# Kernel optimization log

Measured on AMD Instinct MI355X. Metric: run time of the kernel, lower is better.

The kernel has to match this reference:

```python
import jax, jax.numpy as jnp
import numpy as np

# 8 trilerp corners in (x, y, z) component order, matching the original's
# [floor/ceil] enumeration: fff, ffc, fcf, fcc, cff, cfc, ccf, ccc.
CORNERS = np.array([[0, 0, 0], [0, 0, 1], [0, 1, 0], [0, 1, 1],
                    [1, 0, 0], [1, 0, 1], [1, 1, 0], [1, 1, 1]], dtype=np.int32)

N = 32768          # number of points
NUM_KERNELS = 4    # submodels
GRID = 16          # voxel grid size
C_IN = 64          # input_channels
C_OUT = 64         # features


def setup_inputs() -> dict:
    key = jax.random.key(0)
    k1, k2, k3, k4, k5 = jax.random.split(key, 5)
    param_idxs = jax.random.randint(k1, (N, 1), 0, NUM_KERNELS, dtype=jnp.int32)
    pos = jax.random.uniform(k2, (N, 3), dtype=jnp.float32)
    xs = jax.random.normal(k3, (N, C_IN), dtype=jnp.float32)
    # he_uniform over fan_in = input_channels
    limit = np.sqrt(6.0 / C_IN).astype(np.float32)
    kernels = jax.random.uniform(
        k4, (NUM_KERNELS, GRID, GRID, GRID, C_IN, C_OUT),
        dtype=jnp.float32, minval=-limit, maxval=limit)
    biases = jnp.zeros((NUM_KERNELS, GRID, GRID, GRID, C_OUT), dtype=jnp.float32)
    return {"param_idxs": param_idxs, "pos": pos, "xs": xs,
            "kernels": kernels, "biases": biases}


def reference(param_idxs, pos, xs, kernels, biases):
    """Trilinearly-interpolated per-point dense layer.

    Equivalent to building kernel = sum_c w_c * K_c and computing x @ kernel + bias;
    by linearity we accumulate w_c * (x @ K_c + b_c) directly, avoiding the
    materialized per-point interpolated kernel.
    """
    grid = kernels.shape[1]
    pidx = param_idxs.reshape(-1)            # (N,)
    loc = pos * grid - 0.5                    # (N, 3)
    floored = jnp.floor(loc)
    ceil_w = loc - floored                    # trilerp weights toward ceil
    floor_w = 1.0 - ceil_w
    out = jnp.zeros((pos.shape[0], kernels.shape[-1]), dtype=xs.dtype)
    for corner in CORNERS:                    # fixed 8-iteration loop
        idx = jnp.clip((floored + corner).astype(jnp.int32), 0, grid - 1)  # (N,3)
        w = jnp.prod(jnp.where(corner[None, :] == 1, ceil_w, floor_w), axis=-1)  # (N,)
        # Original indexes kernels[pidx, z, y, x] with z=idx[:,2], y=idx[:,1], x=idx[:,0]
        gk = kernels[pidx, idx[:, 2], idx[:, 1], idx[:, 0]]  # (N, C_in, C_out)
        gb = biases[pidx, idx[:, 2], idx[:, 1], idx[:, 0]]   # (N, C_out)
        out = out + w[:, None] * (jnp.einsum('nc,ncf->nf', xs, gk) + gb)
    return out
```

## Files before the change

kernel.cpp:

```cpp
#include <hip/hip_runtime.h>
#include <math.h>

#define NPTS   32768
#define NK     4
#define GRID_  16
#define CIN    64
#define COUT   64
#define NCELLS (NK*GRID_*GRID_*GRID_)
#define NENT   (NPTS*8)
#define NENTP  (NENT + NCELLS*15)
#define CPB    16

typedef __attribute__((ext_vector_type(8))) short  short8;
typedef __attribute__((ext_vector_type(4))) float  f32x4;

static __device__ inline unsigned short f2bf(float f) {
    unsigned int u = __builtin_bit_cast(unsigned int, f);
    unsigned int r = u + 0x7fff + ((u >> 16) & 1);
    return (unsigned short)(r >> 16);
}

__global__ void k_hist(const int* __restrict__ pidx, const float* __restrict__ pos,
                       int* __restrict__ hist, int n) {
    int p = blockIdx.x * blockDim.x + threadIdx.x;
    if (p >= n) return;
    int pk = pidx[p];
    float lx = pos[3*p+0]*16.f - 0.5f;
    float ly = pos[3*p+1]*16.f - 0.5f;
    float lz = pos[3*p+2]*16.f - 0.5f;
    int fx = (int)floorf(lx), fy = (int)floorf(ly), fz = (int)floorf(lz);
#pragma unroll
    for (int c = 0; c < 8; ++c) {
        int c0 = c & 1, c1 = (c >> 1) & 1, c2 = (c >> 2) & 1;
        int ix = min(max(fx + c0, 0), GRID_-1);
        int iy = min(max(fy + c1, 0), GRID_-1);
        int iz = min(max(fz + c2, 0), GRID_-1);
        int cell = ((pk*GRID_ + iz)*GRID_ + iy)*GRID_ + ix;
        atomicAdd(&hist[cell], 1);
    }
}

__global__ void k_alloc(const int* __restrict__ hist, int* __restrict__ offsets,
                        int* __restrict__ cursor, int* __restrict__ gcnt) {
    int i = blockIdx.x * blockDim.x + threadIdx.x;
    int l = threadIdx.x & 63;
    int v  = hist[i];
    int vp = (v + 15) & ~15;
    int p = vp;
#pragma unroll
    for (int d = 1; d < 64; d <<= 1) {
        int t = __shfl_up(p, d);
        if (l >= d) p += t;
    }
    int total = __shfl(p, 63);
    int base = 0;
    if (l == 63) base = atomicAdd(gcnt, total);
    base = __shfl(base, 63);
    int off = base + p - vp;
    offsets[i] = off;
    cursor[i]  = off;
}

__global__ void k_scatter(const int* __restrict__ pidx, const float* __restrict__ pos,
                          int* __restrict__ cursor, int* __restrict__ epid,
                          float* __restrict__ ew, int n) {
    int p = blockIdx.x * blockDim.x + threadIdx.x;
    if (p >= n) return;
    int pk = pidx[p];
    float lx = pos[3*p+0]*16.f - 0.5f;
    float ly = pos[3*p+1]*16.f - 0.5f;
    float lz = pos[3*p+2]*16.f - 0.5f;
    float flx = floorf(lx), fly = floorf(ly), flz = floorf(lz);
    int fx = (int)flx, fy = (int)fly, fz = (int)flz;
    float tx = lx - flx, ty = ly - fly, tz = lz - flz;
    float wx[2] = {1.f - tx, tx};
    float wy[2] = {1.f - ty, ty};
    float wz[2] = {1.f - tz, tz};
#pragma unroll
    for (int c = 0; c < 8; ++c) {
        int c0 = c & 1, c1 = (c >> 1) & 1, c2 = (c >> 2) & 1;
        int ix = min(max(fx + c0, 0), GRID_-1);
        int iy = min(max(fy + c1, 0), GRID_-1);
        int iz = min(max(fz + c2, 0), GRID_-1);
        int cell = ((pk*GRID_ + iz)*GRID_ + iy)*GRID_ + ix;
        float w = wx[c0] * wy[c1] * wz[c2];
        int e = atomicAdd(&cursor[cell], 1);
        epid[e] = p;
        ew[e]   = w;
    }
}

__global__ __launch_bounds__(256)
void k_main(const float* __restrict__ xs, const float* __restrict__ kernels,
            const float* __restrict__ biases, const int* __restrict__ offsets,
            const int* __restrict__ hist, const int* __restrict__ epid,
            const float* __restrict__ ew, float* __restrict__ out) {
    __shared__ float Ks[2][CIN * COUT];
    int tid = threadIdx.x;
    int l   = tid & 63;
    int wv  = tid >> 6;
    int m16 = l & 15;
    int q   = l >> 4;
    int cell0 = blockIdx.x * CPB;
    int ncol  = wv * 16 + m16;

    {
        const float* Kg = kernels + (size_t)cell0 * (CIN * COUT);
#pragma unroll
        for (int r = 0; r < 4; ++r) {
            int off = ((r * 4 + wv) * 64 + l) * 4;
            __builtin_amdgcn_global_load_lds(
                (const __attribute__((address_space(1))) void*)(Kg + off),
                (__attribute__((address_space(3))) void*)(&Ks[0][off]), 16, 0, 0);
        }
    }

    for (int ci = 0; ci < CPB; ++ci) {
        int cur = ci & 1;
        __syncthreads();
        if (ci + 1 < CPB) {
            const float* Kg = kernels + (size_t)(cell0 + ci + 1) * (CIN * COUT);
#pragma unroll
            for (int r = 0; r < 4; ++r) {
                int off = ((r * 4 + wv) * 64 + l) * 4;
                __builtin_amdgcn_global_load_lds(
                    (const __attribute__((address_space(1))) void*)(Kg + off),
                    (__attribute__((address_space(3))) void*)(&Ks[1 - cur][off]), 16, 0, 0);
            }
        }
        int cell = cell0 + ci;
        int cnt  = hist[cell];
        if (cnt == 0) continue;
        int start = offsets[cell];

        short8 Bf0, Bf1;
#pragma unroll
        for (int j = 0; j < 8; ++j) {
            Bf0[j] = (short)f2bf(Ks[cur][(q * 8 + j) * COUT + ncol]);
            Bf1[j] = (short)f2bf(Ks[cur][(32 + q * 8 + j) * COUT + ncol]);
        }
        float bias_c = biases[(size_t)cell * COUT + ncol];

        int nb = (cnt + 15) >> 4;
        for (int b = 0; b < nb; ++b) {
            int ebase = start + (b << 4);
            int pidA = epid[ebase + m16] & (NPTS - 1);
            const float* xr = xs + (size_t)pidA * CIN + q * 8;
            float4 a0 = *(const float4*)(xr);
            float4 a1 = *(const float4*)(xr + 4);
            float4 a2 = *(const float4*)(xr + 32);
            float4 a3 = *(const float4*)(xr + 36);
            short8 af0, af1;
            af0[0]=(short)f2bf(a0.x); af0[1]=(short)f2bf(a0.y);
            af0[2]=(short)f2bf(a0.z); af0[3]=(short)f2bf(a0.w);
            af0[4]=(short)f2bf(a1.x); af0[5]=(short)f2bf(a1.y);
            af0[6]=(short)f2bf(a1.z); af0[7]=(short)f2bf(a1.w);
            af1[0]=(short)f2bf(a2.x); af1[1]=(short)f2bf(a2.y);
            af1[2]=(short)f2bf(a2.z); af1[3]=(short)f2bf(a2.w);
            af1[4]=(short)f2bf(a3.x); af1[5]=(short)f2bf(a3.y);
            af1[6]=(short)f2bf(a3.z); af1[7]=(short)f2bf(a3.w);

            f32x4 acc = {0.f, 0.f, 0.f, 0.f};
            acc = __builtin_amdgcn_mfma_f32_16x16x32_bf16(af0, Bf0, acc, 0, 0, 0);
            acc = __builtin_amdgcn_mfma_f32_16x16x32_bf16(af1, Bf1, acc, 0, 0, 0);

            int erow = ebase + (q << 2);
            int4   pe = *(const int4*)&epid[erow];
            float4 we = *(const float4*)&ew[erow];
            int rem = cnt - (b << 4) - (q << 2);
            if (rem > 0) {
                unsafeAtomicAdd(&out[(size_t)(pe.x) * COUT + ncol], we.x * (acc[0] + bias_c));
                if (rem > 1) unsafeAtomicAdd(&out[(size_t)(pe.y) * COUT + ncol], we.y * (acc[1] + bias_c));
                if (rem > 2) unsafeAtomicAdd(&out[(size_t)(pe.z) * COUT + ncol], we.z * (acc[2] + bias_c));
                if (rem > 3) unsafeAtomicAdd(&out[(size_t)(pe.w) * COUT + ncol], we.w * (acc[3] + bias_c));
            }
        }
    }
}

extern "C" void kernel_launch(void* const* d_in, const int* in_sizes, int n_in,
                              void* d_out, int out_size, void* d_ws, size_t ws_size,
                              hipStream_t stream) {
    const int*   pidx    = (const int*)  d_in[0];
    const float* pos     = (const float*)d_in[1];
    const float* xs      = (const float*)d_in[2];
    const float* kernels = (const float*)d_in[3];
    const float* biases  = (const float*)d_in[4];
    float*       out     = (float*)d_out;
    int n = in_sizes[0];

    int* ws      = (int*)d_ws;
    int* hist    = ws;
    int* gcnt    = ws + NCELLS;
    int* offsets = ws + NCELLS + 16;
    int* cursor  = offsets + NCELLS;
    int* epid    = cursor + NCELLS;
    float* ew    = (float*)(epid + NENTP);

    hipMemsetAsync(hist, 0, (NCELLS + 16) * sizeof(int), stream);
    hipMemsetAsync(d_out, 0, (size_t)out_size * sizeof(float), stream);

    int blocks = (n + 255) / 256;
    k_hist   <<<blocks,       256, 0, stream>>>(pidx, pos, hist, n);
    k_alloc  <<<NCELLS / 256, 256, 0, stream>>>(hist, offsets, cursor, gcnt);
    k_scatter<<<blocks,       256, 0, stream>>>(pidx, pos, cursor, epid, ew, n);
    k_main   <<<NCELLS / CPB, 256, 0, stream>>>(xs, kernels, biases, offsets,
                                                hist, epid, ew, out);
}
```

Before: 442.0 us.

## Replace atomic output accumulation with per-corner result buffer and reduction kernel

The main kernel now writes each corner's unweighted result (x@K + b) to a per-entry buffer indexed by point*8+corner instead of atomically adding weighted results into the output. A new final kernel does the 8-corner weighted reduction per point, which removes the output memset and the float atomics. The main kernel also switches to one cell per block without K double-buffering, and stages the gathered x rows through shared memory in bf16. In exchange it writes and rereads a 32768*8*64 float intermediate (64 MB), adds a launch, and loses the cross-cell prefetch overlap.

```diff
diff --git a/kernel.cpp b/kernel.cpp
--- a/kernel.cpp
+++ b/kernel.cpp
@@ -9,7 +9,6 @@
 #define NCELLS (NK*GRID_*GRID_*GRID_)
 #define NENT   (NPTS*8)
 #define NENTP  (NENT + NCELLS*15)
-#define CPB    16
 
 typedef __attribute__((ext_vector_type(8))) short  short8;
 typedef __attribute__((ext_vector_type(4))) float  f32x4;
@@ -56,13 +55,12 @@
     int base = 0;
     if (l == 63) base = atomicAdd(gcnt, total);
     base = __shfl(base, 63);
-    int off = base + p - vp;
-    offsets[i] = off;
-    cursor[i]  = off;
+    offsets[i] = base + p - vp;
+    cursor[i]  = base + p - vp;
 }
 
 __global__ void k_scatter(const int* __restrict__ pidx, const float* __restrict__ pos,
-                          int* __restrict__ cursor, int* __restrict__ epid,
+                          int* __restrict__ cursor, int* __restrict__ ebuf,
                           float* __restrict__ ew, int n) {
     int p = blockIdx.x * blockDim.x + threadIdx.x;
     if (p >= n) return;
@@ -83,99 +81,105 @@
         int iy = min(max(fy + c1, 0), GRID_-1);
         int iz = min(max(fz + c2, 0), GRID_-1);
         int cell = ((pk*GRID_ + iz)*GRID_ + iy)*GRID_ + ix;
-        float w = wx[c0] * wy[c1] * wz[c2];
+        ew[p * 8 + c] = wx[c0] * wy[c1] * wz[c2];
         int e = atomicAdd(&cursor[cell], 1);
-        epid[e] = p;
-        ew[e]   = w;
+        ebuf[e] = p * 8 + c;
     }
 }
 
 __global__ __launch_bounds__(256)
 void k_main(const float* __restrict__ xs, const float* __restrict__ kernels,
             const float* __restrict__ biases, const int* __restrict__ offsets,
-            const int* __restrict__ hist, const int* __restrict__ epid,
-            const float* __restrict__ ew, float* __restrict__ out) {
-    __shared__ float Ks[2][CIN * COUT];
+            const int* __restrict__ hist, const int* __restrict__ ebuf,
+            float* __restrict__ res) {
+    __shared__ float Ks[CIN * COUT];
+    __shared__ unsigned short Xb[16 * 72];
+    __shared__ int eB[16];
+
+    int cell = blockIdx.x;
+    int cnt  = hist[cell];
+    if (cnt == 0) return;
+    int start = offsets[cell];
+
     int tid = threadIdx.x;
     int l   = tid & 63;
     int wv  = tid >> 6;
     int m16 = l & 15;
     int q   = l >> 4;
-    int cell0 = blockIdx.x * CPB;
-    int ncol  = wv * 16 + m16;
-
-    {
-        const float* Kg = kernels + (size_t)cell0 * (CIN * COUT);
-#pragma unroll
-        for (int r = 0; r < 4; ++r) {
-            int off = ((r * 4 + wv) * 64 + l) * 4;
-            __builtin_amdgcn_global_load_lds(
-                (const __attribute__((address_space(1))) void*)(Kg + off),
-                (__attribute__((address_space(3))) void*)(&Ks[0][off]), 16, 0, 0);
+    int ncol = wv * 16 + m16;
+
+    const float* Kg = kernels + (size_t)cell * (CIN * COUT);
+#pragma unroll
+    for (int r = 0; r < 4; ++r) {
+        int off = ((r * 4 + wv) * 64 + l) * 4;
+        __builtin_amdgcn_global_load_lds(
+            (const __attribute__((address_space(1))) void*)(Kg + off),
+            (__attribute__((address_space(3))) void*)(&Ks[off]), 16, 0, 0);
+    }
+    float bias_c = biases[(size_t)cell * COUT + ncol];
+    __syncthreads();
+
+    short8 Bf0, Bf1;
+#pragma unroll
+    for (int j = 0; j < 8; ++j) {
+        Bf0[j] = (short)f2bf(Ks[(q * 8 + j) * COUT + ncol]);
+        Bf1[j] = (short)f2bf(Ks[(32 + q * 8 + j) * COUT + ncol]);
+    }
+
+    int nb = (cnt + 15) >> 4;
+    for (int b = 0; b < nb; ++b) {
+        int ebase = start + (b << 4);
+        {
+            int row = tid >> 4;
+            int c4  = (tid & 15) << 2;
+            int eid = ebuf[ebase + row] & (NENT - 1);
+            int pid = eid >> 3;
+            float4 xv = *(const float4*)&xs[(size_t)pid * CIN + c4];
+            ushort4 xb = { f2bf(xv.x), f2bf(xv.y), f2bf(xv.z), f2bf(xv.w) };
+            *(ushort4*)&Xb[row * 72 + c4] = xb;
+            if (tid < 16) eB[tid] = ebuf[ebase + tid] & (NENT - 1);
         }
-    }
-
-    for (int ci = 0; ci < CPB; ++ci) {
-        int cur = ci & 1;
         __syncthreads();
-        if (ci + 1 < CPB) {
-            const float* Kg = kernels + (size_t)(cell0 + ci + 1) * (CIN * COUT);
-#pragma unroll
-            for (int r = 0; r < 4; ++r) {
-                int off = ((r * 4 + wv) * 64 + l) * 4;
-                __builtin_amdgcn_global_load_lds(
-                    (const __attribute__((address_space(1))) void*)(Kg + off),
-                    (__attribute__((address_space(3))) void*)(&Ks[1 - cur][off]), 16, 0, 0);
+
+        f32x4 acc = {0.f, 0.f, 0.f, 0.f};
+        {
+            const short8 af0 = *(const short8*)&Xb[m16 * 72 + q * 8];
+            const short8 af1 = *(const short8*)&Xb[m16 * 72 + 32 + q * 8];
+            acc = __builtin_amdgcn_mfma_f32_16x16x32_bf16(af0, Bf0, acc, 0, 0, 0);
+            acc = __builtin_amdgcn_mfma_f32_16x16x32_bf16(af1, Bf1, acc, 0, 0, 0);
+        }
+
+        int valid = cnt - (b << 4);
+#pragma unroll
+        for (int reg = 0; reg < 4; ++reg) {
+            int row = (q << 2) + reg;
+            if (row < valid) {
+                int eid = eB[row];
+                res[(size_t)eid * COUT + ncol] = acc[reg] + bias_c;
             }
         }
-        int cell = cell0 + ci;
-        int cnt  = hist[cell];
-        if (cnt == 0) continue;
-        int start = offsets[cell];
-
-        short8 Bf0, Bf1;
-#pragma unroll
-        for (int j = 0; j < 8; ++j) {
-            Bf0[j] = (short)f2bf(Ks[cur][(q * 8 + j) * COUT + ncol]);
-            Bf1[j] = (short)f2bf(Ks[cur][(32 + q * 8 + j) * COUT + ncol]);
-        }
-        float bias_c = biases[(size_t)cell * COUT + ncol];
-
-        int nb = (cnt + 15) >> 4;
-        for (int b = 0; b < nb; ++b) {
-            int ebase = start + (b << 4);
-            int pidA = epid[ebase + m16] & (NPTS - 1);
-            const float* xr = xs + (size_t)pidA * CIN + q * 8;
-            float4 a0 = *(const float4*)(xr);
-            float4 a1 = *(const float4*)(xr + 4);
-            float4 a2 = *(const float4*)(xr + 32);
-            float4 a3 = *(const float4*)(xr + 36);
-            short8 af0, af1;
-            af0[0]=(short)f2bf(a0.x); af0[1]=(short)f2bf(a0.y);
-            af0[2]=(short)f2bf(a0.z); af0[3]=(short)f2bf(a0.w);
-            af0[4]=(short)f2bf(a1.x); af0[5]=(short)f2bf(a1.y);
-            af0[6]=(short)f2bf(a1.z); af0[7]=(short)f2bf(a1.w);
-            af1[0]=(short)f2bf(a2.x); af1[1]=(short)f2bf(a2.y);
-            af1[2]=(short)f2bf(a2.z); af1[3]=(short)f2bf(a2.w);
-            af1[4]=(short)f2bf(a3.x); af1[5]=(short)f2bf(a3.y);
-            af1[6]=(short)f2bf(a3.z); af1[7]=(short)f2bf(a3.w);
-
-            f32x4 acc = {0.f, 0.f, 0.f, 0.f};
-            acc = __builtin_amdgcn_mfma_f32_16x16x32_bf16(af0, Bf0, acc, 0, 0, 0);
-            acc = __builtin_amdgcn_mfma_f32_16x16x32_bf16(af1, Bf1, acc, 0, 0, 0);
-
-            int erow = ebase + (q << 2);
-            int4   pe = *(const int4*)&epid[erow];
-            float4 we = *(const float4*)&ew[erow];
-            int rem = cnt - (b << 4) - (q << 2);
-            if (rem > 0) {
-                unsafeAtomicAdd(&out[(size_t)(pe.x) * COUT + ncol], we.x * (acc[0] + bias_c));
-                if (rem > 1) unsafeAtomicAdd(&out[(size_t)(pe.y) * COUT + ncol], we.y * (acc[1] + bias_c));
-                if (rem > 2) unsafeAtomicAdd(&out[(size_t)(pe.z) * COUT + ncol], we.z * (acc[2] + bias_c));
-                if (rem > 3) unsafeAtomicAdd(&out[(size_t)(pe.w) * COUT + ncol], we.w * (acc[3] + bias_c));
-            }
-        }
-    }
+        __syncthreads();
+    }
+}
+
+__global__ __launch_bounds__(256)
+void k_final(const float* __restrict__ res, const float* __restrict__ ew,
+             float* __restrict__ out, int n) {
+    int tid = threadIdx.x;
+    int p   = blockIdx.x * 16 + (tid >> 4);
+    if (p >= n) return;
+    int c4  = (tid & 15) << 2;
+    f32x4 acc = {0.f, 0.f, 0.f, 0.f};
+#pragma unroll
+    for (int c = 0; c < 8; ++c) {
+        float w = ew[p * 8 + c];
+        const float4 r = *(const float4*)&res[(size_t)(p * 8 + c) * COUT + c4];
+        acc[0] = fmaf(w, r.x, acc[0]);
+        acc[1] = fmaf(w, r.y, acc[1]);
+        acc[2] = fmaf(w, r.z, acc[2]);
+        acc[3] = fmaf(w, r.w, acc[3]);
+    }
+    *(float4*)&out[(size_t)p * COUT + c4] = *(float4*)&acc;
 }
 
 extern "C" void kernel_launch(void* const* d_in, const int* in_sizes, int n_in,
@@ -194,16 +198,17 @@
     int* gcnt    = ws + NCELLS;
     int* offsets = ws + NCELLS + 16;
     int* cursor  = offsets + NCELLS;
-    int* epid    = cursor + NCELLS;
-    float* ew    = (float*)(epid + NENTP);
+    int* ebuf    = cursor + NCELLS;
+    float* ew    = (float*)(ebuf + NENTP);
+    float* res   = ew + NENT;
 
     hipMemsetAsync(hist, 0, (NCELLS + 16) * sizeof(int), stream);
-    hipMemsetAsync(d_out, 0, (size_t)out_size * sizeof(float), stream);
 
     int blocks = (n + 255) / 256;
     k_hist   <<<blocks,       256, 0, stream>>>(pidx, pos, hist, n);
     k_alloc  <<<NCELLS / 256, 256, 0, stream>>>(hist, offsets, cursor, gcnt);
-    k_scatter<<<blocks,       256, 0, stream>>>(pidx, pos, cursor, epid, ew, n);
-    k_main   <<<NCELLS / CPB, 256, 0, stream>>>(xs, kernels, biases, offsets,
-                                                hist, epid, ew, out);
-}
+    k_scatter<<<blocks,       256, 0, stream>>>(pidx, pos, cursor, ebuf, ew, n);
+    k_main   <<<NCELLS,       256, 0, stream>>>(xs, kernels, biases, offsets,
+                                                hist, ebuf, res);
+    k_final  <<<(n + 15) / 16, 256, 0, stream>>>(res, ew, out, n);
+}
```

After: 431.0 us. -2.5%, faster.
